# Kernel optimization log

Hardware: AMD Instinct MI355X
Metric: run time of the kernel (lower is better)

Reference implementation:

```python
import jax, jax.numpy as jnp
import numpy as np

BATCH, H, W = 1024, 32, 32
NUM_PIXELS = H * W                 # 1024
NUM_WIRES = 11                     # ceil(log2(1024)) + 1
NUM_LAYERS = 8

_CNOT = jnp.array([[1, 0, 0, 0],
                   [0, 1, 0, 0],
                   [0, 0, 0, 1],
                   [0, 0, 1, 0]], dtype=jnp.complex64)


def setup_inputs() -> dict:
    key = jax.random.key(0)
    k1, k2, k3 = jax.random.split(key, 3)
    image = jax.random.uniform(k1, (BATCH, 1, H, W), dtype=jnp.float32)
    label = jax.random.normal(k2, (BATCH,), dtype=jnp.float32)
    weights = jax.random.normal(k3, (NUM_LAYERS, NUM_WIRES, 3), dtype=jnp.float32) * 0.4
    return {"image": image, "label": label, "weights": weights}


def _apply_1q(state, U, w):
    # state: (B,) + (2,)*n ; U: (2,2) shared or (B,2,2) per-batch
    st = jnp.moveaxis(state, w + 1, -1)
    if U.ndim == 3:
        out = jnp.einsum('bij,b...j->b...i', U, st)
    else:
        out = jnp.einsum('ij,...j->...i', U, st)
    return jnp.moveaxis(out, -1, w + 1)


def _apply_cnot(state, c, t):
    last = state.ndim - 1
    st = jnp.moveaxis(state, (c + 1, t + 1), (last - 1, last))
    sh = st.shape
    st = st.reshape(sh[:-2] + (4,)) @ _CNOT.T
    st = st.reshape(sh)
    return jnp.moveaxis(st, (last - 1, last), (c + 1, t + 1))


def _rot(phi, theta, omega):
    # PennyLane Rot = RZ(omega) RY(theta) RZ(phi)
    c = jnp.cos(theta / 2).astype(jnp.complex64)
    s = jnp.sin(theta / 2).astype(jnp.complex64)
    ep = jnp.exp(-0.5j * (phi + omega))
    em = jnp.exp(0.5j * (phi - omega))
    return jnp.array([[ep * c, -em * s],
                      [jnp.conj(em) * s, jnp.conj(ep) * c]])


def _circuit(image, label, weights):
    B = image.shape[0]
    x = image.reshape(B, NUM_PIXELS)
    # AmplitudeEmbedding(normalize=True) on wires 0..NUM_WIRES-2; ancilla wire in |0>
    psi = x / jnp.linalg.norm(x, axis=1, keepdims=True)
    state = jnp.zeros((B, 2 ** NUM_WIRES), jnp.complex64)
    state = state.at[:, ::2].set(psi.astype(jnp.complex64))  # ancilla = least-significant wire
    state = state.reshape((B,) + (2,) * NUM_WIRES)

    # RX(label) on the last wire (per-batch angle)
    c = jnp.cos(label / 2).astype(jnp.complex64)
    s = (-1j * jnp.sin(label / 2)).astype(jnp.complex64)
    rx = jnp.stack([jnp.stack([c, s], -1), jnp.stack([s, c], -1)], -2)  # (B,2,2)
    state = _apply_1q(state, rx, NUM_WIRES - 1)

    # weights remapped as in the module
    wr = jnp.pi * jnp.tanh(weights)

    # StronglyEntanglingLayers: per layer, Rot on every wire then ring of CNOTs with range r
    for l in range(NUM_LAYERS):
        for q in range(NUM_WIRES):
            state = _apply_1q(state, _rot(wr[l, q, 0], wr[l, q, 1], wr[l, q, 2]), q)
        r = (l % (NUM_WIRES - 1)) + 1
        for q in range(NUM_WIRES):
            state = _apply_cnot(state, q, (q + r) % NUM_WIRES)

    probs = jnp.abs(state.reshape(B, -1)) ** 2          # (B, 2048)
    probs = probs[:, ::2]                               # ancilla == 0 outcomes, (B, 1024)
    out = probs * NUM_PIXELS                            # decode: undo 1/num_pixels scale
    return out.reshape(B, 1, H, W)


def reference(image, label, weights):
    return _circuit(image, label, weights)
```

## Files before the change

### kernel.cpp

```cpp
#include <hip/hip_runtime.h>
#include <math.h>

#define NW 11
#define NL 8
#define NPIX 1024
#define TPB 256

typedef float f2 __attribute__((ext_vector_type(2)));
typedef float f4 __attribute__((ext_vector_type(4)));

struct PermTab { int fe[NL][8]; int d[NL][8]; };

__host__ __device__ inline int fmap_h(int m, int r) {
    for (int q = 0; q < NW; ++q) {
        int pc = 10 - q;
        int qq = q + r; if (qq >= NW) qq -= NW;
        int pt = 10 - qq;
        m ^= ((m >> pc) & 1) << pt;
    }
    return m;
}

__host__ __device__ constexpr int SW(int e) {
    return e ^ (((e >> 3) & 7) << 1) ^ (((e >> 6) & 1) << 3);
}

template<int B>
__device__ __forceinline__ void gate8(f2 (&v)[8], const f2* __restrict__ g) {
    f2 c0 = g[0], c1 = g[1], c2 = g[2], c3 = g[3];
    f2 c4 = g[4], c5 = g[5], c6 = g[6], c7 = g[7];
    #pragma unroll
    for (int s = 0; s < 8; ++s) {
        if (s & B) continue;
        f2 v0 = v[s], v1 = v[s | B];
        f2 w0 = v0.yx, w1 = v1.yx;
        f2 o0 = __builtin_elementwise_fma(c3, w1,
                 __builtin_elementwise_fma(c2, v1,
                  __builtin_elementwise_fma(c1, w0, c0 * v0)));
        f2 o1 = __builtin_elementwise_fma(c7, w1,
                 __builtin_elementwise_fma(c6, v1,
                  __builtin_elementwise_fma(c5, w0, c4 * v0)));
        v[s] = o0; v[s | B] = o1;
    }
}

__global__ void gates_kernel(const float* __restrict__ weights, f2* __restrict__ gw) {
    int t = threadIdx.x;
    if (t < NL * NW) {
        const float* w = weights + t * 3;
        const float PI = 3.14159265358979323846f;
        float phi   = PI * tanhf(w[0]);
        float theta = PI * tanhf(w[1]);
        float omega = PI * tanhf(w[2]);
        float ct = cosf(0.5f * theta), st = sinf(0.5f * theta);
        float a  = 0.5f * (phi + omega), bb = 0.5f * (phi - omega);
        float ca = cosf(a), sa = sinf(a), cb = cosf(bb), sb = sinf(bb);
        float u00r =  ca * ct, u00i = -sa * ct;
        float u01r = -cb * st, u01i = -sb * st;
        float u10r =  cb * st, u10i = -sb * st;
        float u11r =  ca * ct, u11i =  sa * ct;
        f2* g = gw + t * 8;
        g[0] = (f2){u00r, u00r}; g[1] = (f2){-u00i, u00i};
        g[2] = (f2){u01r, u01r}; g[3] = (f2){-u01i, u01i};
        g[4] = (f2){u10r, u10r}; g[5] = (f2){-u10i, u10i};
        g[6] = (f2){u11r, u11r}; g[7] = (f2){-u11i, u11i};
    }
}

__global__ __launch_bounds__(TPB) void pqc_kernel(
    const float* __restrict__ image, const float* __restrict__ label,
    const f2* __restrict__ gw, float* __restrict__ out, PermTab pt)
{
    __shared__ __align__(16) f2 sS[2048];
    __shared__ float sRed[4];

    const int b = blockIdx.x, t = threadIdx.x;

    const f4 x = ((const f4*)(image + (size_t)b * NPIX))[t];
    float ss = x.x * x.x + x.y * x.y + x.z * x.z + x.w * x.w;
    #pragma unroll
    for (int off = 32; off >= 1; off >>= 1) ss += __shfl_down(ss, off);
    if ((t & 63) == 0) sRed[t >> 6] = ss;
    __syncthreads();
    const float inv = 1.0f / sqrtf(sRed[0] + sRed[1] + sRed[2] + sRed[3]);

    const float lab = label[b];
    const float cl = cosf(0.5f * lab), sl = sinf(0.5f * lab);

    f2 v[8];
    {
        float ps[4] = {x.x, x.y, x.z, x.w};
        #pragma unroll
        for (int m = 0; m < 4; ++m) {
            float p = ps[m] * inv;
            v[2 * m]     = (f2){cl * p, 0.f};
            v[2 * m + 1] = (f2){0.f, -sl * p};
        }
    }

    const int swb0 = SW(t << 3);
    const int swb1 = SW((t & 7) | ((t >> 3) << 6));
    const int swb2 = SW((t & 63) | ((t >> 6) << 9));
    const int swb3 = SW(t << 1);

    for (int l = 0; l < NL; ++l) {
        const f2* G = gw + (size_t)l * NW * 8;

        if (l) {
            #pragma unroll
            for (int k = 0; k < 4; ++k) {
                f4 w = *(const f4*)&sS[swb0 ^ SW(2 * k)];
                v[2 * k] = w.xy; v[2 * k + 1] = w.zw;
            }
        }
        gate8<1>(v, G + 10 * 8);
        gate8<2>(v, G +  9 * 8);
        gate8<4>(v, G +  8 * 8);
        #pragma unroll
        for (int k = 0; k < 4; ++k) {
            f4 w; w.xy = v[2 * k]; w.zw = v[2 * k + 1];
            *(f4*)&sS[swb0 ^ SW(2 * k)] = w;
        }
        __syncthreads();

        {
            #pragma unroll
            for (int s = 0; s < 8; ++s) v[s] = sS[swb1 ^ SW(s << 3)];
            gate8<1>(v, G + 7 * 8);
            gate8<2>(v, G + 6 * 8);
            gate8<4>(v, G + 5 * 8);
            #pragma unroll
            for (int s = 0; s < 8; ++s) sS[swb1 ^ SW(s << 3)] = v[s];
        }
        __syncthreads();

        {
            #pragma unroll
            for (int s = 0; s < 8; ++s) v[s] = sS[swb2 ^ SW(s << 6)];
            gate8<1>(v, G + 4 * 8);
            gate8<2>(v, G + 3 * 8);
            gate8<4>(v, G + 2 * 8);
            #pragma unroll
            for (int s = 0; s < 8; ++s) sS[swb2 ^ SW(s << 6)] = v[s];
        }
        __syncthreads();

        {
            #pragma unroll
            for (int k = 0; k < 4; ++k) {
                f4 w = *(const f4*)&sS[swb3 ^ ((k & 1) << 9) ^ ((k >> 1) << 10)];
                v[2 * k] = w.xy; v[2 * k + 1] = w.zw;
            }
            gate8<2>(v, G + 1 * 8);
            gate8<4>(v, G + 0 * 8);
            int msw = 0;
            #pragma unroll
            for (int k2 = 0; k2 < 8; ++k2)
                msw ^= ((t >> k2) & 1) ? pt.fe[l][k2] : 0;
            #pragma unroll
            for (int s = 0; s < 8; ++s) sS[msw ^ pt.d[l][s]] = v[s];
        }
        __syncthreads();
    }

    {
        f4 o;
        #pragma unroll
        for (int k = 0; k < 4; ++k) {
            f2 a = sS[swb0 ^ SW(2 * k)];
            ((float*)&o)[k] = (a.x * a.x + a.y * a.y) * (float)NPIX;
        }
        ((f4*)(out + (size_t)b * NPIX))[t] = o;
    }
}

extern "C" void kernel_launch(void* const* d_in, const int* in_sizes, int n_in,
                              void* d_out, int out_size, void* d_ws, size_t ws_size,
                              hipStream_t stream) {
    const float* image   = (const float*)d_in[0];
    const float* label   = (const float*)d_in[1];
    const float* weights = (const float*)d_in[2];
    float* out = (float*)d_out;
    f2* gw = (f2*)d_ws;

    PermTab pt;
    for (int l = 0; l < NL; ++l) {
        int r = l + 1;
        for (int k = 0; k < 8; ++k)
            pt.fe[l][k] = SW(fmap_h(1 << (k + 1), r));
        for (int s = 0; s < 8; ++s) {
            int m = 0;
            if (s & 1) m ^= fmap_h(1,       r);
            if (s & 2) m ^= fmap_h(1 << 9,  r);
            if (s & 4) m ^= fmap_h(1 << 10, r);
            pt.d[l][s] = SW(m);
        }
    }

    int batch = in_sizes[1];
    gates_kernel<<<1, 128, 0, stream>>>(weights, gw);
    pqc_kernel<<<batch, TPB, 0, stream>>>(image, label, gw, out, pt);
}
```

Measured before the change: 45.06 us.

## Simulate each circuit in one wavefront with register-resident state and cross-lane gates

The kernel now runs each batch element in a single 64-lane wavefront that holds 32 amplitudes per lane in registers. Gates on high wires act within registers, while gates on lane-index wires use DPP, permlane32 swaps and shuffles instead of round trips through shared memory. The CNOT permutation goes through LDS once per layer with only a waitcnt instead of block barriers. The gate matrices are computed inside the kernel, which removes the separate gates kernel launch. In exchange there is much higher register pressure and only one wave per block, and every block recomputes the gate table.

```diff
diff --git a/kernel.cpp b/kernel.cpp
--- a/kernel.cpp
+++ b/kernel.cpp
@@ -4,14 +4,13 @@
 #define NW 11
 #define NL 8
 #define NPIX 1024
-#define TPB 256
 
 typedef float f2 __attribute__((ext_vector_type(2)));
 typedef float f4 __attribute__((ext_vector_type(4)));
 
-struct PermTab { int fe[NL][8]; int d[NL][8]; };
-
-__host__ __device__ inline int fmap_h(int m, int r) {
+struct FTab { int C[NL][NW]; };
+
+static inline int fmap_h(int m, int r) {
     for (int q = 0; q < NW; ++q) {
         int pc = 10 - q;
         int qq = q + r; if (qq >= NW) qq -= NW;
@@ -21,32 +20,84 @@
     return m;
 }
 
-__host__ __device__ constexpr int SW(int e) {
-    return e ^ (((e >> 3) & 7) << 1) ^ (((e >> 6) & 1) << 3);
-}
-
-template<int B>
-__device__ __forceinline__ void gate8(f2 (&v)[8], const f2* __restrict__ g) {
-    f2 c0 = g[0], c1 = g[1], c2 = g[2], c3 = g[3];
-    f2 c4 = g[4], c5 = g[5], c6 = g[6], c7 = g[7];
-    #pragma unroll
-    for (int s = 0; s < 8; ++s) {
-        if (s & B) continue;
-        f2 v0 = v[s], v1 = v[s | B];
-        f2 w0 = v0.yx, w1 = v1.yx;
-        f2 o0 = __builtin_elementwise_fma(c3, w1,
-                 __builtin_elementwise_fma(c2, v1,
-                  __builtin_elementwise_fma(c1, w0, c0 * v0)));
-        f2 o1 = __builtin_elementwise_fma(c7, w1,
-                 __builtin_elementwise_fma(c6, v1,
-                  __builtin_elementwise_fma(c5, w0, c4 * v0)));
-        v[s] = o0; v[s | B] = o1;
-    }
-}
-
-__global__ void gates_kernel(const float* __restrict__ weights, f2* __restrict__ gw) {
-    int t = threadIdx.x;
-    if (t < NL * NW) {
+#define FMA2 __builtin_elementwise_fma
+
+template<int CTRL>
+__device__ __forceinline__ float dpp_f(float x) {
+    int xi = __float_as_int(x);
+    int r  = __builtin_amdgcn_update_dpp(xi, xi, CTRL, 0xF, 0xF, false);
+    return __int_as_float(r);
+}
+template<int CTRL>
+__device__ __forceinline__ f2 dpp2(f2 v) {
+    return (f2){dpp_f<CTRL>(v.x), dpp_f<CTRL>(v.y)};
+}
+
+template<int MODE>
+__device__ __forceinline__ f2 bfetch(f2 v, int L) {
+    if constexpr (MODE == 0) return dpp2<0x128>(v);
+    else if constexpr (MODE == 1) {
+        f2 fwd = dpp2<0x104>(v);
+        f2 bwd = dpp2<0x114>(v);
+        return (L & 4) ? bwd : fwd;
+    }
+    else if constexpr (MODE == 2) return dpp2<0x4E>(v);
+    else return dpp2<0xB1>(v);
+}
+
+__device__ __forceinline__ void swap32(f2& a, f2& b) {
+    float ax = a.x, ay = a.y, bx = b.x, by = b.y;
+    asm volatile("v_permlane32_swap_b32 %0, %1" : "+v"(ax), "+v"(bx));
+    asm volatile("v_permlane32_swap_b32 %0, %1" : "+v"(ay), "+v"(by));
+    a = (f2){ax, ay}; b = (f2){bx, by};
+}
+__device__ __forceinline__ void swapX(f2& a, f2& b, bool hi, int mask) {
+    float sx = hi ? a.x : b.x;
+    float sy = hi ? a.y : b.y;
+    f2 t = (f2){__shfl_xor(sx, mask, 64), __shfl_xor(sy, mask, 64)};
+    a = hi ? t : a;
+    b = hi ? b : t;
+}
+
+template<int M>
+__device__ __forceinline__ void gateR(f2 (&X)[32], const f2* __restrict__ g) {
+    const f2 c0 = g[0], c1 = g[1], c2 = g[2], c3 = g[3];
+    const f2 c4 = g[4], c5 = g[5], c6 = g[6], c7 = g[7];
+    #pragma unroll
+    for (int s = 0; s < 32; ++s) {
+        if (s & M) continue;
+        const int s1 = s | M;
+        f2 v0 = X[s], v1 = X[s1];
+        f2 v0y = v0.yx, v1y = v1.yx;
+        X[s]  = FMA2(c3, v1y, FMA2(c2, v1, FMA2(c1, v0y, c0 * v0)));
+        X[s1] = FMA2(c7, v1y, FMA2(c6, v1, FMA2(c5, v0y, c4 * v0)));
+    }
+}
+
+template<int LBIT, int MODE>
+__device__ __forceinline__ void gateL(f2 (&X)[32], const f2* __restrict__ g, int L) {
+    const bool sb = (L >> LBIT) & 1;
+    const f2 a0 = sb ? g[6] : g[0], a1 = sb ? g[7] : g[1];
+    const f2 b0 = sb ? g[4] : g[2], b1 = sb ? g[5] : g[3];
+    #pragma unroll
+    for (int s = 0; s < 32; ++s) {
+        f2 v = X[s];
+        f2 p = bfetch<MODE>(v, L);
+        f2 vy = v.yx, py = p.yx;
+        X[s] = FMA2(b1, py, FMA2(b0, p, FMA2(a1, vy, a0 * v)));
+    }
+}
+
+__global__ __launch_bounds__(64) void pqc_kernel(
+    const float* __restrict__ image, const float* __restrict__ label,
+    const float* __restrict__ weights, float* __restrict__ out, FTab ft)
+{
+    __shared__ __align__(16) f2 sS[2048];
+    __shared__ __align__(16) f2 sG[NL * NW * 8];
+
+    const int b = blockIdx.x, L = threadIdx.x;
+
+    for (int t = L; t < NL * NW; t += 64) {
         const float* w = weights + t * 3;
         const float PI = 3.14159265358979323846f;
         float phi   = PI * tanhf(w[0]);
@@ -55,122 +106,100 @@
         float ct = cosf(0.5f * theta), st = sinf(0.5f * theta);
         float a  = 0.5f * (phi + omega), bb = 0.5f * (phi - omega);
         float ca = cosf(a), sa = sinf(a), cb = cosf(bb), sb = sinf(bb);
-        float u00r =  ca * ct, u00i = -sa * ct;
-        float u01r = -cb * st, u01i = -sb * st;
-        float u10r =  cb * st, u10i = -sb * st;
-        float u11r =  ca * ct, u11i =  sa * ct;
-        f2* g = gw + t * 8;
-        g[0] = (f2){u00r, u00r}; g[1] = (f2){-u00i, u00i};
-        g[2] = (f2){u01r, u01r}; g[3] = (f2){-u01i, u01i};
-        g[4] = (f2){u10r, u10r}; g[5] = (f2){-u10i, u10i};
-        g[6] = (f2){u11r, u11r}; g[7] = (f2){-u11i, u11i};
-    }
-}
-
-__global__ __launch_bounds__(TPB) void pqc_kernel(
-    const float* __restrict__ image, const float* __restrict__ label,
-    const f2* __restrict__ gw, float* __restrict__ out, PermTab pt)
-{
-    __shared__ __align__(16) f2 sS[2048];
-    __shared__ float sRed[4];
-
-    const int b = blockIdx.x, t = threadIdx.x;
-
-    const f4 x = ((const f4*)(image + (size_t)b * NPIX))[t];
-    float ss = x.x * x.x + x.y * x.y + x.z * x.z + x.w * x.w;
-    #pragma unroll
-    for (int off = 32; off >= 1; off >>= 1) ss += __shfl_down(ss, off);
-    if ((t & 63) == 0) sRed[t >> 6] = ss;
-    __syncthreads();
-    const float inv = 1.0f / sqrtf(sRed[0] + sRed[1] + sRed[2] + sRed[3]);
+        f2* g = sG + t * 8;
+        g[0] = (f2){ ca * ct,  ca * ct};  g[1] = (f2){ sa * ct,  -sa * ct};
+        g[2] = (f2){-cb * st, -cb * st};  g[3] = (f2){ sb * st,  -sb * st};
+        g[4] = (f2){ cb * st,  cb * st};  g[5] = (f2){ sb * st,  -sb * st};
+        g[6] = (f2){ ca * ct,  ca * ct};  g[7] = (f2){-sa * ct,   sa * ct};
+    }
+
+    float* psi = (float*)sS;
+    const f4* img4 = (const f4*)(image + (size_t)b * NPIX);
+    f4 xs[4];
+    float ss = 0.f;
+    #pragma unroll
+    for (int k = 0; k < 4; ++k) {
+        xs[k] = img4[L + 64 * k];
+        ss += xs[k].x * xs[k].x + xs[k].y * xs[k].y
+            + xs[k].z * xs[k].z + xs[k].w * xs[k].w;
+    }
+    #pragma unroll
+    for (int o = 32; o >= 1; o >>= 1) ss += __shfl_xor(ss, o, 64);
+    const float inv = 1.0f / sqrtf(ss);
+    #pragma unroll
+    for (int k = 0; k < 4; ++k) *(f4*)&psi[(L + 64 * k) * 4] = xs[k];
+    asm volatile("s_waitcnt lgkmcnt(0)" ::: "memory");
 
     const float lab = label[b];
-    const float cl = cosf(0.5f * lab), sl = sinf(0.5f * lab);
-
-    f2 v[8];
-    {
-        float ps[4] = {x.x, x.y, x.z, x.w};
-        #pragma unroll
-        for (int m = 0; m < 4; ++m) {
-            float p = ps[m] * inv;
-            v[2 * m]     = (f2){cl * p, 0.f};
-            v[2 * m + 1] = (f2){0.f, -sl * p};
+    const float clp =  cosf(0.5f * lab) * inv;
+    const float slp = -sinf(0.5f * lab) * inv;
+    const bool odd = L & 1;
+    f2 X[32];
+    #pragma unroll
+    for (int j = 0; j < 32; ++j) {
+        float pv = psi[(j << 5) | (L >> 1)];
+        X[j] = odd ? (f2){0.f, slp * pv} : (f2){clp * pv, 0.f};
+    }
+    asm volatile("s_waitcnt lgkmcnt(0)" ::: "memory");
+
+    const bool hi4 = (L >> 4) & 1;
+
+    for (int l = 0; l < NL; ++l) {
+        const f2* G = sG + l * NW * 8;
+
+        gateR<16>(X, G + 0 * 8);
+        gateR< 8>(X, G + 1 * 8);
+        gateR< 4>(X, G + 2 * 8);
+        gateR< 2>(X, G + 3 * 8);
+        gateR< 1>(X, G + 4 * 8);
+
+        #pragma unroll
+        for (int j = 0; j < 16; ++j) swap32(X[j], X[j + 16]);
+        gateR<16>(X, G + 5 * 8);
+
+        #pragma unroll
+        for (int jj = 0; jj < 16; ++jj) {
+            int j = (jj & 7) | ((jj >> 3) << 4);
+            swapX(X[j], X[j + 8], hi4, 16);
         }
-    }
-
-    const int swb0 = SW(t << 3);
-    const int swb1 = SW((t & 7) | ((t >> 3) << 6));
-    const int swb2 = SW((t & 63) | ((t >> 6) << 9));
-    const int swb3 = SW(t << 1);
-
-    for (int l = 0; l < NL; ++l) {
-        const f2* G = gw + (size_t)l * NW * 8;
-
-        if (l) {
-            #pragma unroll
-            for (int k = 0; k < 4; ++k) {
-                f4 w = *(const f4*)&sS[swb0 ^ SW(2 * k)];
-                v[2 * k] = w.xy; v[2 * k + 1] = w.zw;
-            }
+        gateR<8>(X, G + 6 * 8);
+
+        gateL<3, 0>(X, G + 7 * 8, L);
+        gateL<2, 1>(X, G + 8 * 8, L);
+        gateL<1, 2>(X, G + 9 * 8, L);
+        gateL<0, 3>(X, G + 10 * 8, L);
+
+        const int* C = ft.C[l];
+        int FL = 0;
+        FL ^= ((L >> 5) & 1) ? C[10] : 0;
+        FL ^= ((L >> 4) & 1) ? C[9]  : 0;
+        FL ^= ((L >> 3) & 1) ? C[3]  : 0;
+        FL ^= ((L >> 2) & 1) ? C[2]  : 0;
+        FL ^= ((L >> 1) & 1) ? C[1]  : 0;
+        FL ^= ( L       & 1) ? C[0]  : 0;
+        const int c5 = C[5], c4 = C[4], c8 = C[8], c7 = C[7], c6 = C[6];
+        #pragma unroll
+        for (int j = 0; j < 32; ++j) {
+            int fr = ((j & 16) ? c5 : 0) ^ ((j & 8) ? c4 : 0)
+                   ^ ((j & 4)  ? c8 : 0) ^ ((j & 2) ? c7 : 0)
+                   ^ ((j & 1)  ? c6 : 0);
+            sS[FL ^ fr] = X[j];
         }
-        gate8<1>(v, G + 10 * 8);
-        gate8<2>(v, G +  9 * 8);
-        gate8<4>(v, G +  8 * 8);
-        #pragma unroll
-        for (int k = 0; k < 4; ++k) {
-            f4 w; w.xy = v[2 * k]; w.zw = v[2 * k + 1];
-            *(f4*)&sS[swb0 ^ SW(2 * k)] = w;
+        asm volatile("s_waitcnt lgkmcnt(0)" ::: "memory");
+        __builtin_amdgcn_sched_barrier(0);
+        #pragma unroll
+        for (int j = 0; j < 32; ++j) X[j] = sS[(j << 6) | L];
+        asm volatile("s_waitcnt lgkmcnt(0)" ::: "memory");
+        __builtin_amdgcn_sched_barrier(0);
+    }
+
+    if (!odd) {
+        float* ob = out + (size_t)b * NPIX + (L >> 1);
+        #pragma unroll
+        for (int j = 0; j < 32; ++j) {
+            f2 a = X[j];
+            ob[j << 5] = (a.x * a.x + a.y * a.y) * (float)NPIX;
         }
-        __syncthreads();
-
-        {
-            #pragma unroll
-            for (int s = 0; s < 8; ++s) v[s] = sS[swb1 ^ SW(s << 3)];
-            gate8<1>(v, G + 7 * 8);
-            gate8<2>(v, G + 6 * 8);
-            gate8<4>(v, G + 5 * 8);
-            #pragma unroll
-            for (int s = 0; s < 8; ++s) sS[swb1 ^ SW(s << 3)] = v[s];
-        }
-        __syncthreads();
-
-        {
-            #pragma unroll
-            for (int s = 0; s < 8; ++s) v[s] = sS[swb2 ^ SW(s << 6)];
-            gate8<1>(v, G + 4 * 8);
-            gate8<2>(v, G + 3 * 8);
-            gate8<4>(v, G + 2 * 8);
-            #pragma unroll
-            for (int s = 0; s < 8; ++s) sS[swb2 ^ SW(s << 6)] = v[s];
-        }
-        __syncthreads();
-
-        {
-            #pragma unroll
-            for (int k = 0; k < 4; ++k) {
-                f4 w = *(const f4*)&sS[swb3 ^ ((k & 1) << 9) ^ ((k >> 1) << 10)];
-                v[2 * k] = w.xy; v[2 * k + 1] = w.zw;
-            }
-            gate8<2>(v, G + 1 * 8);
-            gate8<4>(v, G + 0 * 8);
-            int msw = 0;
-            #pragma unroll
-            for (int k2 = 0; k2 < 8; ++k2)
-                msw ^= ((t >> k2) & 1) ? pt.fe[l][k2] : 0;
-            #pragma unroll
-            for (int s = 0; s < 8; ++s) sS[msw ^ pt.d[l][s]] = v[s];
-        }
-        __syncthreads();
-    }
-
-    {
-        f4 o;
-        #pragma unroll
-        for (int k = 0; k < 4; ++k) {
-            f2 a = sS[swb0 ^ SW(2 * k)];
-            ((float*)&o)[k] = (a.x * a.x + a.y * a.y) * (float)NPIX;
-        }
-        ((f4*)(out + (size_t)b * NPIX))[t] = o;
     }
 }
 
@@ -181,23 +210,12 @@
     const float* label   = (const float*)d_in[1];
     const float* weights = (const float*)d_in[2];
     float* out = (float*)d_out;
-    f2* gw = (f2*)d_ws;
-
-    PermTab pt;
-    for (int l = 0; l < NL; ++l) {
-        int r = l + 1;
-        for (int k = 0; k < 8; ++k)
-            pt.fe[l][k] = SW(fmap_h(1 << (k + 1), r));
-        for (int s = 0; s < 8; ++s) {
-            int m = 0;
-            if (s & 1) m ^= fmap_h(1,       r);
-            if (s & 2) m ^= fmap_h(1 << 9,  r);
-            if (s & 4) m ^= fmap_h(1 << 10, r);
-            pt.d[l][s] = SW(m);
-        }
-    }
+
+    FTab ft;
+    for (int l = 0; l < NL; ++l)
+        for (int bpos = 0; bpos < NW; ++bpos)
+            ft.C[l][bpos] = fmap_h(1 << bpos, l + 1);
 
     int batch = in_sizes[1];
-    gates_kernel<<<1, 128, 0, stream>>>(weights, gw);
-    pqc_kernel<<<batch, TPB, 0, stream>>>(image, label, gw, out, pt);
-}
+    pqc_kernel<<<batch, 64, 0, stream>>>(image, label, weights, out, ft);
+}
```

Result: slower. 60.93 us (+35.2%).
